# Kernel optimization log

Measured on AMD Instinct MI355X. Metric: run time of the kernel, lower is better.

Reference implementation:

```python
import jax, jax.numpy as jnp
import numpy as np

EPS = 1e-12  # F.normalize eps
CLAMP = 30.0
POS_W = 1.0
NEG_W = 1.0
LABEL_SMOOTHING = 0.0


def _l2_normalize(x):
    n = jnp.sqrt(jnp.sum(x * x, axis=-1, keepdims=True))
    return x / jnp.maximum(n, EPS)


def setup_inputs() -> dict:
    key = jax.random.key(0)
    kv, kt = jax.random.split(key)
    B, D = 8192, 512
    video_features = jax.random.normal(kv, (B, D), dtype=jnp.float32)
    text_features = jax.random.normal(kt, (B, D), dtype=jnp.float32)
    log_temp = jnp.asarray(np.log(0.07), dtype=jnp.float32)  # typical CLIP init
    bias = jnp.asarray(-10.0, dtype=jnp.float32)  # bias_init
    return {
        "video_features": video_features,
        "text_features": text_features,
        "log_temp": log_temp,
        "bias": bias,
    }


def reference(video_features, text_features, log_temp, bias):
    v = _l2_normalize(video_features.astype(jnp.float32))  # [B_v, D]
    t = _l2_normalize(text_features.astype(jnp.float32))   # [B_t, D]
    sim = jnp.einsum("vd,td->vt", v, t)                    # [B_v, B_t]
    temp = jnp.exp(log_temp.astype(jnp.float32))
    logits = jnp.clip(sim / temp + bias, -CLAMP, CLAMP)
    B_v, B_t = v.shape[0], t.shape[0]
    m = min(B_v, B_t)
    # diagonal positive labels (pos_mask is None path)
    labels = jnp.zeros((B_v, B_t), jnp.float32).at[jnp.arange(m), jnp.arange(m)].set(1.0)
    if LABEL_SMOOTHING > 0:
        labels = labels * (1 - LABEL_SMOOTHING) + LABEL_SMOOTHING / 2
    weights = jnp.where(labels > 0.5, POS_W, NEG_W).astype(jnp.float32)
    # numerically stable BCE-with-logits, elementwise then weighted mean
    z = logits
    bce = jnp.maximum(z, 0.0) - z * labels + jnp.log1p(jnp.exp(-jnp.abs(z)))
    return jnp.mean(weights * bce)
```

## Files before the change

### kernel.cpp

```cpp
#include <hip/hip_runtime.h>
#include <cstdint>

#define NB 8192
#define ND 512
#define BM 256
#define BN 256
#define BK 32
#define NTL (ND / BK)
#define THREADS 512
#define BUFS 16384

typedef __bf16 bf16x8 __attribute__((ext_vector_type(8)));
typedef float f32x4 __attribute__((ext_vector_type(4)));

__device__ __forceinline__ unsigned short f2bf(float f) {
    union { float f; uint32_t u; } c; c.f = f;
    return (unsigned short)((c.u + 0x7fffu + ((c.u >> 16) & 1u)) >> 16);
}

__device__ __forceinline__ void load16(const void* g, void* l) {
    __builtin_amdgcn_global_load_lds(
        (void __attribute__((address_space(1)))*)(const_cast<void*>(g)),
        (void __attribute__((address_space(3)))*)(l),
        16, 0, 0);
}

__global__ __launch_bounds__(256) void norm_cast(const float* __restrict__ v,
                                                 const float* __restrict__ t,
                                                 unsigned short* __restrict__ vn,
                                                 unsigned short* __restrict__ tn,
                                                 int ns) {
    const int wave = threadIdx.x >> 6;
    const int lane = threadIdx.x & 63;
    const int row = blockIdx.x * 4 + wave;
    const float* src;
    unsigned short* dst;
    if (row < NB) { src = v + (size_t)row * ND; dst = vn + (size_t)row * ns; }
    else { src = t + (size_t)(row - NB) * ND; dst = tn + (size_t)(row - NB) * ns; }
    float4 a = ((const float4*)src)[lane * 2];
    float4 b = ((const float4*)src)[lane * 2 + 1];
    float ss = a.x * a.x + a.y * a.y + a.z * a.z + a.w * a.w
             + b.x * b.x + b.y * b.y + b.z * b.z + b.w * b.w;
#pragma unroll
    for (int off = 32; off; off >>= 1) ss += __shfl_xor(ss, off);
    const float sc = 1.0f / fmaxf(sqrtf(ss), 1e-12f);
    union { unsigned short us[8]; uint4 q; } pk;
    pk.us[0] = f2bf(a.x * sc); pk.us[1] = f2bf(a.y * sc);
    pk.us[2] = f2bf(a.z * sc); pk.us[3] = f2bf(a.w * sc);
    pk.us[4] = f2bf(b.x * sc); pk.us[5] = f2bf(b.y * sc);
    pk.us[6] = f2bf(b.z * sc); pk.us[7] = f2bf(b.w * sc);
    ((uint4*)dst)[lane] = pk.q;
}

__global__ __launch_bounds__(THREADS, 2) void gemm_bce(const unsigned short* __restrict__ vn,
                                                       const unsigned short* __restrict__ tn,
                                                       const float* __restrict__ lt,
                                                       const float* __restrict__ bp,
                                                       float* __restrict__ out_sum,
                                                       int ns) {
    __shared__ __align__(16) unsigned short smem[3 * BUFS];
    __shared__ float red[8];

    const int tid = threadIdx.x;
    const int lane = tid & 63;
    const int wave = tid >> 6;
    const int wr = wave >> 2;
    const int wc = wave & 3;
    const int lq = lane & 15;
    const int lh = lane >> 4;

    const int m0 = (int)(blockIdx.x >> 5) * BM;
    const int n0 = (int)(blockIdx.x & 31) * BN;

    const int schunk = ((lane & 3) ^ ((lane >> 3) & 3)) * 8;
    const unsigned short* sA = vn + (size_t)(m0 + 32 * wave + (lane >> 2)) * ns + schunk;
    const unsigned short* sB = tn + (size_t)(n0 + 32 * wave + (lane >> 2)) * ns + schunk;

#define STG(T, B) do {                                                         \
        unsigned short* _dA = smem + (B) * BUFS + wave * 1024;                 \
        unsigned short* _dB = _dA + 8192;                                      \
        load16(sA + (T) * 32, _dA);                                            \
        load16(sA + (T) * 32 + (size_t)16 * ns, _dA + 512);                    \
        load16(sB + (T) * 32, _dB);                                            \
        load16(sB + (T) * 32 + (size_t)16 * ns, _dB + 512);                    \
    } while (0)

    const int sl = (lh ^ ((lq >> 1) & 3)) * 8;
    const int aro = (wr * 16 + lq) * 32 + sl;
    const int bro = (wc * 16 + lq) * 32 + sl;
#define RD_A(C, M) (*(const bf16x8*)(smem + (C) * BUFS + aro + (M) * 1024))
#define RD_B(C, N) (*(const bf16x8*)(smem + (C) * BUFS + 8192 + bro + (N) * 2048))

#define BAR __builtin_amdgcn_s_barrier()
#define SCB __builtin_amdgcn_sched_barrier(0)
#define VM4 asm volatile("s_waitcnt vmcnt(4)" ::: "memory")
#define VM0 asm volatile("s_waitcnt vmcnt(0)" ::: "memory")

    f32x4 acc[8][4];
#pragma unroll
    for (int m = 0; m < 8; ++m)
#pragma unroll
        for (int n = 0; n < 4; ++n)
            acc[m][n] = f32x4{0.f, 0.f, 0.f, 0.f};

    bf16x8 afr[8], bfr[4];

#define TILE(T, S, WMODE) do {                                                  \
                                       \
        _Pragma("unroll") for (int mm = 0; mm < 4; ++mm) afr[mm] = RD_A((T) % 3, mm); \
        _Pragma("unroll") for (int nn = 0; nn < 4; ++nn) bfr[nn] = RD_B((T) % 3, nn); \
        SCB;                                                                    \
           \
        _Pragma("unroll") for (int mm = 4; mm < 8; ++mm) afr[mm] = RD_A((T) % 3, mm); \
        if (S) STG((T) + 2, ((T) + 2) % 3);                                     \
        SCB;                                                                    \
        __builtin_amdgcn_s_setprio(1);                                          \
        _Pragma("unroll") for (int mm = 0; mm < 4; ++mm)                        \
        _Pragma("unroll") for (int nn = 0; nn < 4; ++nn)                        \
            acc[mm][nn] = __builtin_amdgcn_mfma_f32_16x16x32_bf16(              \
                afr[mm], bfr[nn], acc[mm][nn], 0, 0, 0);                        \
        __builtin_amdgcn_s_setprio(0); SCB;                                     \
        __builtin_amdgcn_s_setprio(1);                                          \
        _Pragma("unroll") for (int mm = 4; mm < 8; ++mm)                        \
        _Pragma("unroll") for (int nn = 0; nn < 4; ++nn)                        \
            acc[mm][nn] = __builtin_amdgcn_mfma_f32_16x16x32_bf16(              \
                afr[mm], bfr[nn], acc[mm][nn], 0, 0, 0);                        \
        __builtin_amdgcn_s_setprio(0); SCB;                                     \
        if ((WMODE) == 0) { VM4; BAR; SCB; }                                    \
        else if ((WMODE) == 1) { VM0; BAR; SCB; }                               \
    } while (0)

    STG(0, 0);
    STG(1, 1);
    VM4; BAR; SCB;

    TILE(0,  true, 0);  TILE(1,  true, 0);  TILE(2,  true, 0);  TILE(3,  true, 0);
    TILE(4,  true, 0);  TILE(5,  true, 0);  TILE(6,  true, 0);  TILE(7,  true, 0);
    TILE(8,  true, 0);  TILE(9,  true, 0);  TILE(10, true, 0);  TILE(11, true, 0);
    TILE(12, true, 0);  TILE(13, true, 0);  TILE(14, false, 1); TILE(15, false, 2);

    const float invtemp = __expf(-lt[0]);
    const float bias = bp[0];
    float local = 0.f;
    const int row_base = m0 + wr * 16 + lh * 4;
    const int col_base = n0 + wc * 16 + lq;
#pragma unroll
    for (int m = 0; m < 8; ++m) {
#pragma unroll
        for (int n = 0; n < 4; ++n) {
#pragma unroll
            for (int r = 0; r < 4; ++r) {
                const float s = acc[m][n][r];
                float z = fminf(fmaxf(fmaf(s, invtemp, bias), -30.f), 30.f);
                const int gr = row_base + m * 32 + r;
                const int gc = col_base + n * 64;
                local += fmaxf(z, 0.f) + __logf(1.0f + __expf(-fabsf(z))) - ((gr == gc) ? z : 0.f);
            }
        }
    }
#pragma unroll
    for (int off = 32; off; off >>= 1) local += __shfl_xor(local, off);
    if (lane == 0) red[wave] = local;
    __syncthreads();
    if (tid == 0) {
        float tot = 0.f;
#pragma unroll
        for (int w = 0; w < 8; ++w) tot += red[w];
        atomicAdd(out_sum, tot * (1.0f / 67108864.0f));
    }
}

extern "C" void kernel_launch(void* const* d_in, const int* in_sizes, int n_in,
                              void* d_out, int out_size, void* d_ws, size_t ws_size,
                              hipStream_t stream) {
    const float* v = (const float*)d_in[0];
    const float* t = (const float*)d_in[1];
    const float* lt = (const float*)d_in[2];
    const float* bp = (const float*)d_in[3];
    float* out = (float*)d_out;

    const size_t need = (size_t)2 * NB * ND * sizeof(unsigned short);
    unsigned short *vn, *tn;
    int ns;
    if (ws_size >= need) {
        vn = (unsigned short*)d_ws;
        tn = vn + (size_t)NB * ND;
        ns = ND;
    } else {
        vn = (unsigned short*)d_in[0];
        tn = (unsigned short*)d_in[1];
        ns = ND * 2;
    }

    hipMemsetAsync(out, 0, sizeof(float), stream);
    hipLaunchKernelGGL(norm_cast, dim3((2 * NB) / 4), dim3(256), 0, stream, v, t, vn, tn, ns);
    hipLaunchKernelGGL(gemm_bce, dim3((NB / BM) * (NB / BN)), dim3(THREADS), 0, stream,
                       vn, tn, lt, bp, out, ns);
}
```

Baseline: 176.3 us.

## Switch GEMM to double-buffered LDS with register-fragment ping-pong prefetch

Replaces the triple-buffered LDS pipeline with two LDS buffers plus two sets of register fragments, so the fragments for the next K-tile are read from LDS while the current tile's MFMAs run. The global-to-LDS stage for tile T+2 is issued into the buffer just drained, and each tile ends with a full vmcnt(0) wait and barrier. Launch bounds drop to one block per CU-slot hint, which lets the compiler use more registers for the doubled fragments but may reduce occupancy. The full vmcnt(0) wait each tile also cuts how far global loads can run ahead.

```diff
diff --git a/kernel.cpp b/kernel.cpp
--- a/kernel.cpp
+++ b/kernel.cpp
@@ -6,7 +6,6 @@
 #define BM 256
 #define BN 256
 #define BK 32
-#define NTL (ND / BK)
 #define THREADS 512
 #define BUFS 16384
 
@@ -52,13 +51,13 @@
     ((uint4*)dst)[lane] = pk.q;
 }
 
-__global__ __launch_bounds__(THREADS, 2) void gemm_bce(const unsigned short* __restrict__ vn,
+__global__ __launch_bounds__(THREADS, 1) void gemm_bce(const unsigned short* __restrict__ vn,
                                                        const unsigned short* __restrict__ tn,
                                                        const float* __restrict__ lt,
                                                        const float* __restrict__ bp,
                                                        float* __restrict__ out_sum,
                                                        int ns) {
-    __shared__ __align__(16) unsigned short smem[3 * BUFS];
+    __shared__ __align__(16) unsigned short smem[2 * BUFS];
     __shared__ float red[8];
 
     const int tid = threadIdx.x;
@@ -93,7 +92,7 @@
 
 #define BAR __builtin_amdgcn_s_barrier()
 #define SCB __builtin_amdgcn_sched_barrier(0)
-#define VM4 asm volatile("s_waitcnt vmcnt(4)" ::: "memory")
+#define LGK0 asm volatile("s_waitcnt lgkmcnt(0)" ::: "memory")
 #define VM0 asm volatile("s_waitcnt vmcnt(0)" ::: "memory")
 
     f32x4 acc[8][4];
@@ -103,41 +102,52 @@
         for (int n = 0; n < 4; ++n)
             acc[m][n] = f32x4{0.f, 0.f, 0.f, 0.f};
 
-    bf16x8 afr[8], bfr[4];
-
-#define TILE(T, S, WMODE) do {                                                  \
-                                       \
-        _Pragma("unroll") for (int mm = 0; mm < 4; ++mm) afr[mm] = RD_A((T) % 3, mm); \
-        _Pragma("unroll") for (int nn = 0; nn < 4; ++nn) bfr[nn] = RD_B((T) % 3, nn); \
+    bf16x8 afrX[8], bfrX[4], afrY[8], bfrY[4];
+
+#define RD12(AF, BF, BUF) do {                                                  \
+        _Pragma("unroll") for (int mm = 0; mm < 8; ++mm) AF[mm] = RD_A(BUF, mm); \
+        _Pragma("unroll") for (int nn = 0; nn < 4; ++nn) BF[nn] = RD_B(BUF, nn); \
+    } while (0)
+
+#define MFMAH(AF, BF, MB)                                                       \
+    _Pragma("unroll") for (int mm = 0; mm < 4; ++mm)                            \
+    _Pragma("unroll") for (int nn = 0; nn < 4; ++nn)                            \
+        acc[(MB) + mm][nn] = __builtin_amdgcn_mfma_f32_16x16x32_bf16(           \
+            AF[(MB) + mm], BF[nn], acc[(MB) + mm][nn], 0, 0, 0)
+
+#define TILE(T, S, R, LAST, AC, BC, AN, BN_) do {                               \
+        LGK0; SCB;       \
+        if (S) STG((T) + 2, (T) & 1);                                           \
+        __builtin_amdgcn_s_setprio(1); MFMAH(AC, BC, 0);                        \
+        __builtin_amdgcn_s_setprio(0); SCB;                                     \
+        if (R) RD12(AN, BN_, ((T) + 1) & 1);                                    \
         SCB;                                                                    \
-           \
-        _Pragma("unroll") for (int mm = 4; mm < 8; ++mm) afr[mm] = RD_A((T) % 3, mm); \
-        if (S) STG((T) + 2, ((T) + 2) % 3);                                     \
-        SCB;                                                                    \
-        __builtin_amdgcn_s_setprio(1);                                          \
-        _Pragma("unroll") for (int mm = 0; mm < 4; ++mm)                        \
-        _Pragma("unroll") for (int nn = 0; nn < 4; ++nn)                        \
-            acc[mm][nn] = __builtin_amdgcn_mfma_f32_16x16x32_bf16(              \
-                afr[mm], bfr[nn], acc[mm][nn], 0, 0, 0);                        \
+        __builtin_amdgcn_s_setprio(1); MFMAH(AC, BC, 4);                        \
         __builtin_amdgcn_s_setprio(0); SCB;                                     \
-        __builtin_amdgcn_s_setprio(1);                                          \
-        _Pragma("unroll") for (int mm = 4; mm < 8; ++mm)                        \
-        _Pragma("unroll") for (int nn = 0; nn < 4; ++nn)                        \
-            acc[mm][nn] = __builtin_amdgcn_mfma_f32_16x16x32_bf16(              \
-                afr[mm], bfr[nn], acc[mm][nn], 0, 0, 0);                        \
-        __builtin_amdgcn_s_setprio(0); SCB;                                     \
-        if ((WMODE) == 0) { VM4; BAR; SCB; }                                    \
-        else if ((WMODE) == 1) { VM0; BAR; SCB; }                               \
+        if (!(LAST)) { VM0; BAR; SCB; }                                         \
     } while (0)
 
     STG(0, 0);
     STG(1, 1);
-    VM4; BAR; SCB;
-
-    TILE(0,  true, 0);  TILE(1,  true, 0);  TILE(2,  true, 0);  TILE(3,  true, 0);
-    TILE(4,  true, 0);  TILE(5,  true, 0);  TILE(6,  true, 0);  TILE(7,  true, 0);
-    TILE(8,  true, 0);  TILE(9,  true, 0);  TILE(10, true, 0);  TILE(11, true, 0);
-    TILE(12, true, 0);  TILE(13, true, 0);  TILE(14, false, 1); TILE(15, false, 2);
+    VM0; BAR; SCB;
+    RD12(afrX, bfrX, 0);
+
+    TILE(0,  1, 1, 0, afrX, bfrX, afrY, bfrY);
+    TILE(1,  1, 1, 0, afrY, bfrY, afrX, bfrX);
+    TILE(2,  1, 1, 0, afrX, bfrX, afrY, bfrY);
+    TILE(3,  1, 1, 0, afrY, bfrY, afrX, bfrX);
+    TILE(4,  1, 1, 0, afrX, bfrX, afrY, bfrY);
+    TILE(5,  1, 1, 0, afrY, bfrY, afrX, bfrX);
+    TILE(6,  1, 1, 0, afrX, bfrX, afrY, bfrY);
+    TILE(7,  1, 1, 0, afrY, bfrY, afrX, bfrX);
+    TILE(8,  1, 1, 0, afrX, bfrX, afrY, bfrY);
+    TILE(9,  1, 1, 0, afrY, bfrY, afrX, bfrX);
+    TILE(10, 1, 1, 0, afrX, bfrX, afrY, bfrY);
+    TILE(11, 1, 1, 0, afrY, bfrY, afrX, bfrX);
+    TILE(12, 1, 1, 0, afrX, bfrX, afrY, bfrY);
+    TILE(13, 1, 1, 0, afrY, bfrY, afrX, bfrX);
+    TILE(14, 0, 1, 0, afrX, bfrX, afrY, bfrY);
+    TILE(15, 0, 0, 1, afrY, bfrY, afrX, bfrX);
 
     const float invtemp = __expf(-lt[0]);
     const float bias = bp[0];
```

Measured after the change: 178.6 us. Within noise of the previous version (+1.3%).
